# Kernel optimization log

Measured on AMD Instinct MI355X. Metric: run time of the kernel, lower is better.

Reference implementation:

```python
import jax, jax.numpy as jnp
import numpy as np

B, C, H, W = 4, 288, 64, 64
P = 2
HEADS = 36
MLP_RATIO = 4.0
D = C * P * P              # hidden_size = 1152
HF = int(D * MLP_RATIO)    # 4608
LN_EPS = 1e-6
ATTN_EPS = 1e-8


def _layernorm(x):
    # LayerNorm over [C,H,W] per sample, no affine
    mu = jnp.mean(x, axis=(1, 2, 3), keepdims=True)
    var = jnp.mean((x - mu) ** 2, axis=(1, 2, 3), keepdims=True)
    return (x - mu) * jax.lax.rsqrt(var + LN_EPS)


def _seg(x):
    # b c (n1 p) (n2 p) -> b (n1 n2) (c p p)
    b, c, h, w = x.shape
    n1, n2 = h // P, w // P
    x = x.reshape(b, c, n1, P, n2, P).transpose(0, 2, 4, 1, 3, 5)
    return x.reshape(b, n1 * n2, c * P * P)


def _comb(t, h, w):
    # b (n1 n2) (c p p) -> b c (n1 p) (n2 p)
    b, n, dd = t.shape
    n1, n2 = h // P, w // P
    c = dd // (P * P)
    x = t.reshape(b, n1, n2, c, P, P).transpose(0, 3, 1, 4, 2, 5)
    return x.reshape(b, c, h, w)


def _lite_la(t, qkv_w, proj_w, proj_b):
    # ReLU-kernel linear attention with ones-padding normalization trick
    b, s, dm = t.shape
    d = dm // HEADS
    qkv = t @ qkv_w.T                       # [b,s,3*dm]
    q, k, v = jnp.split(qkv, 3, axis=-1)
    q = jax.nn.relu(q).reshape(b, s, HEADS, d)
    k = jax.nn.relu(k).reshape(b, s, HEADS, d)
    v = v.reshape(b, s, HEADS, d)
    v = jnp.concatenate([v, jnp.ones((b, s, HEADS, 1), v.dtype)], axis=-1)  # PAD_VAL=1
    vk = jnp.einsum('bshe,bshd->bhed', v, k)       # [b,h,d+1,d]
    out = jnp.einsum('bhed,bshd->bshe', vk, q)     # [b,s,h,d+1]
    out = out[..., :-1] / (out[..., -1:] + ATTN_EPS)
    return out.reshape(b, s, dm) @ proj_w.T + proj_b


def _glumb(t, inv_w, inv_b, dw_w, dw_b, pw_w):
    # GLU MBConv: 1x1 expand + SiLU -> 3x3 depthwise -> GLU gate -> 1x1 project
    b, n, c = t.shape
    hp = wp = int(n ** 0.5)
    x = t.reshape(b, hp, wp, c).transpose(0, 3, 1, 2)  # NCHW
    x = jnp.einsum('bchw,oc->bohw', x, inv_w[:, :, 0, 0]) + inv_b[None, :, None, None]
    x = jax.nn.silu(x)
    x = jax.lax.conv_general_dilated(x, dw_w, (1, 1), 'SAME',
                                     feature_group_count=dw_w.shape[0],
                                     dimension_numbers=('NCHW', 'OIHW', 'NCHW'))
    x = x + dw_b[None, :, None, None]
    x, gate = jnp.split(x, 2, axis=1)
    x = x * jax.nn.silu(gate)
    x = jnp.einsum('bchw,oc->bohw', x, pw_w[:, :, 0, 0])
    return x.reshape(b, c, n).transpose(0, 2, 1)


def setup_inputs() -> dict:
    key = jax.random.key(0)
    ks = jax.random.split(key, 10)
    s = 0.02
    return {
        'x': jax.random.normal(ks[0], (B, C, H, W), jnp.float32),
        'cond': jax.random.normal(ks[1], (B, 6 * C, H, W), jnp.float32),
        'global_token': jax.random.normal(ks[2], (B, D), jnp.float32),
        'time_token': jax.random.normal(ks[3], (B, D), jnp.float32),
        'ss_w': jax.random.normal(ks[4], (6 * C, 6 * C, 1, 1), jnp.float32) * s,
        'ss_b': jnp.zeros((6 * C,), jnp.float32),
        'qkv_w': jax.random.normal(ks[5], (3 * D, D), jnp.float32) * s,
        'proj_w': jax.random.normal(ks[6], (D, D), jnp.float32) * s,
        'proj_b': jnp.zeros((D,), jnp.float32),
        'inv_w': jax.random.normal(ks[7], (2 * HF, D, 1, 1), jnp.float32) * s,
        'inv_b': jnp.zeros((2 * HF,), jnp.float32),
        'dw_w': jax.random.normal(ks[8], (2 * HF, 1, 3, 3), jnp.float32) * s,
        'dw_b': jnp.zeros((2 * HF,), jnp.float32),
        'pw_w': jax.random.normal(ks[9], (D, HF, 1, 1), jnp.float32) * s,
    }


def reference(x, cond, global_token, time_token, ss_w, ss_b, qkv_w, proj_w, proj_b,
              inv_w, inv_b, dw_w, dw_b, pw_w):
    # scale_shift_table: SiLU + 1x1 conv on cond, chunk into 6 per-channel maps
    ss = jnp.einsum('bchw,oc->bohw', jax.nn.silu(cond), ss_w[:, :, 0, 0]) + ss_b[None, :, None, None]
    sh_msa, sc_msa, g_msa, sh_mlp, sc_mlp, g_mlp = jnp.split(ss, 6, axis=1)
    # attention branch
    tok = _seg(_layernorm(x) * (1.0 + sc_msa) + sh_msa)
    tok = jnp.concatenate([global_token[:, None], time_token[:, None], tok], axis=1)
    a = _lite_la(tok, qkv_w, proj_w, proj_b)
    x = x + _comb(a[:, 2:], H, W) * g_msa
    # MLP branch
    m = _glumb(_seg(_layernorm(x) * (1.0 + sc_mlp) + sh_mlp), inv_w, inv_b, dw_w, dw_b, pw_w)
    x = x + _comb(m, H, W) * g_mlp
    return x
```

## Files before the change

kernel.cpp:

```cpp
#include <hip/hip_runtime.h>
#include <hip/hip_bf16.h>
#include <cstdint>


typedef __bf16 bf16;
typedef bf16 bf16x8 __attribute__((ext_vector_type(8)));
typedef bf16 bf16x4 __attribute__((ext_vector_type(4)));
typedef float f32x4 __attribute__((ext_vector_type(4)));

typedef const __attribute__((address_space(1))) void gas_void;
typedef __attribute__((address_space(3))) void las_void;

__device__ __forceinline__ void gload16(const bf16* g, bf16* l) {
    __builtin_amdgcn_global_load_lds((gas_void*)g, (las_void*)l, 16, 0, 0);
}

#define BB 4
#define CC 288
#define HW 4096
#define C6 1728
#define DD 1152
#define SEQ 1026
#define RTOT 4104
#define NTOK 1024
#define HF 4608
#define HF2 9216
#define NPB 1179648

static constexpr size_t OFF_SUMS = 0;
static constexpr size_t OFF_SS   = 256;
static constexpr size_t SS_BYTES = (size_t)C6 * 16384 * 2;
static constexpr size_t OFF_R2   = OFF_SS + SS_BYTES;
static constexpr size_t OFF_PART1= OFF_R2;
static constexpr size_t OFF_A1   = OFF_R2;
static constexpr size_t OFF_T    = OFF_R2;
static constexpr size_t OFF_QKV  = OFF_T   + (size_t)RTOT*DD*2;
static constexpr size_t OFF_PART2= OFF_QKV;
static constexpr size_t OFF_VK   = OFF_QKV + (size_t)3456*RTOT*2;
static constexpr size_t OFF_ATT  = OFF_VK  + (size_t)144*1056*4;
static constexpr size_t OFF_APROJ= OFF_ATT + (size_t)RTOT*DD*2;
static constexpr size_t OFF_T2   = OFF_R2;
static constexpr size_t OFF_Y    = OFF_T2  + (size_t)4096*DD*2;
static constexpr size_t OFF_G    = OFF_Y   + (size_t)4096*HF2*2;
static constexpr size_t OFF_M    = OFF_G   + (size_t)4096*HF*2;
static constexpr size_t OFF_W    = OFF_R2  + 132120576;
static constexpr size_t OFF_WSS  = OFF_W;
static constexpr size_t OFF_WQKV = OFF_WSS  + (size_t)C6*C6*2;
static constexpr size_t OFF_WPROJ= OFF_WQKV + (size_t)3456*DD*2;
static constexpr size_t OFF_WINV = OFF_WPROJ+ (size_t)DD*DD*2;
static constexpr size_t OFF_WPW  = OFF_WINV + (size_t)HF2*DD*2;

__global__ __launch_bounds__(256) void cvt_bf16(const float* __restrict__ s,
                                                bf16* __restrict__ d, int n4) {
    int i = blockIdx.x * 256 + threadIdx.x;
    if (i < n4) {
        float4 v = ((const float4*)s)[i];
        bf16x4 o = {(bf16)v.x, (bf16)v.y, (bf16)v.z, (bf16)v.w};
        ((bf16x4*)d)[i] = o;
    }
}

__device__ __forceinline__ void block_reduce2_store(float s1, float s2, float* dst) {
    #pragma unroll
    for (int o = 32; o > 0; o >>= 1) { s1 += __shfl_down(s1, o); s2 += __shfl_down(s2, o); }
    __shared__ float r1[4], r2[4];
    int wave = threadIdx.x >> 6, lane = threadIdx.x & 63;
    if (lane == 0) { r1[wave] = s1; r2[wave] = s2; }
    __syncthreads();
    if (threadIdx.x == 0) {
        dst[0] = r1[0] + r1[1] + r1[2] + r1[3];
        dst[1] = r2[0] + r2[1] + r2[2] + r2[3];
    }
}

__global__ __launch_bounds__(256) void ln_stats(const float* __restrict__ x, float* __restrict__ part) {
    const float* base = x + (size_t)blockIdx.x * 4096;
    float s1 = 0.f, s2 = 0.f;
    #pragma unroll
    for (int it = 0; it < 4; it++) {
        float4 v = ((const float4*)base)[it * 256 + threadIdx.x];
        s1 += v.x + v.y + v.z + v.w;
        s2 += v.x * v.x + v.y * v.y + v.z * v.z + v.w * v.w;
    }
    block_reduce2_store(s1, s2, part + (size_t)blockIdx.x * 2);
}

__global__ __launch_bounds__(256) void reduce_part(const float* __restrict__ part, float* __restrict__ sums,
                                                   int nper, int out_off) {
    int b = blockIdx.x;
    float s1 = 0.f, s2 = 0.f;
    for (int i = threadIdx.x; i < nper; i += 256) {
        s1 += part[(size_t)(b * nper + i) * 2];
        s2 += part[(size_t)(b * nper + i) * 2 + 1];
    }
    block_reduce2_store(s1, s2, sums + out_off + b * 2);
}

__global__ __launch_bounds__(256) void prep_cond(const float* __restrict__ cond, bf16* __restrict__ A1) {
    __shared__ float tile[64][65];
    int b = blockIdx.z, k0 = blockIdx.y * 64, h0 = blockIdx.x * 64;
    int col = threadIdx.x & 63, r4 = threadIdx.x >> 6;
    const float* src = cond + ((size_t)b * C6 + k0) * HW + h0;
    #pragma unroll
    for (int p = 0; p < 16; p++) {
        int kk = r4 + p * 4;
        float v = src[(size_t)kk * HW + col];
        tile[col][kk] = v / (1.f + __expf(-v));
    }
    __syncthreads();
    bf16* dst = A1 + ((size_t)(b * HW + h0)) * C6 + k0;
    #pragma unroll
    for (int p = 0; p < 16; p++) {
        int rr = r4 + p * 4;
        dst[(size_t)rr * C6 + col] = (bf16)tile[rr][col];
    }
}

template <int EP, int BIAS>
__global__ __launch_bounds__(256) void gemm_bt(const bf16* __restrict__ A, const bf16* __restrict__ B,
                                               const float* __restrict__ bias, bf16* __restrict__ C,
                                               int M, int N, int K, int reluLimit) {
    __shared__ __align__(16) bf16 As[3][128 * 32];
    __shared__ __align__(16) bf16 Bs[3][128 * 32];
    const int tid = threadIdx.x, wave = tid >> 6, lane = tid & 63;

    const int nx = gridDim.x, ny = gridDim.y, G = 8;
    int idx = blockIdx.y * nx + blockIdx.x;
    int total = nx * ny;
    int q = total >> 3, rm = total & 7;
    int xcd = idx & 7, slot = idx >> 3;
    int vid = (xcd < rm ? xcd * (q + 1) : rm * (q + 1) + (xcd - rm) * q) + slot;
    int band = vid / (G * nx);
    int r = vid - band * (G * nx);
    int gm = min(G, ny - band * G);
    const int m0 = (band * G + r % gm) * 128;
    const int n0 = (r / gm) * 128;

    const int c0 = wave * 128 + lane;
    const int c1 = c0 + 64;
    const int sw = ((c0 >> 2) & 3) ^ ((c0 >> 4) & 3);
    const int ka = (((c0 & 3) ^ sw)) * 8;
    int ra0 = min(m0 + (c0 >> 2), M - 1), ra1 = min(m0 + (c1 >> 2), M - 1);
    int rb0 = min(n0 + (c0 >> 2), N - 1), rb1 = min(n0 + (c1 >> 2), N - 1);
    const bf16* gA0 = A + (size_t)ra0 * K + ka;
    const bf16* gA1 = A + (size_t)ra1 * K + ka;
    const bf16* gB0 = B + (size_t)rb0 * K + ka;
    const bf16* gB1 = B + (size_t)rb1 * K + ka;

    const int wm = (wave >> 1) * 64, wn = (wave & 1) * 64;
    const int l15 = lane & 15;
    const int sr = (l15 & 3) ^ ((l15 >> 2) & 3);
    const int fc = ((lane >> 4) ^ sr) * 8;
    const int fao = (wm + l15) * 32 + fc;
    const int fbo = (wn + l15) * 32 + fc;
    const int lwo = wave * 1024;

    f32x4 acc[4][4];
    #pragma unroll
    for (int i = 0; i < 4; i++)
        #pragma unroll
        for (int j = 0; j < 4; j++) acc[i][j] = (f32x4){0.f, 0.f, 0.f, 0.f};

    auto STAGE = [&](int buf) {
        gload16(gA0, &As[buf][lwo]);
        gload16(gA1, &As[buf][lwo + 512]);
        gload16(gB0, &Bs[buf][lwo]);
        gload16(gB1, &Bs[buf][lwo + 512]);
        gA0 += 32; gA1 += 32; gB0 += 32; gB1 += 32;
    };
    auto COMP = [&](int buf) {
        const bf16* fa = &As[buf][fao];
        const bf16* fb = &Bs[buf][fbo];
        bf16x8 af[4], bv[4];
        #pragma unroll
        for (int i = 0; i < 4; i++) af[i] = *(const bf16x8*)(fa + i * 16 * 32);
        #pragma unroll
        for (int j = 0; j < 4; j++) bv[j] = *(const bf16x8*)(fb + j * 16 * 32);
        #pragma unroll
        for (int i = 0; i < 4; i++)
            #pragma unroll
            for (int j = 0; j < 4; j++)
                acc[i][j] = __builtin_amdgcn_mfma_f32_16x16x32_bf16(af[i], bv[j], acc[i][j], 0, 0, 0);
    };
    auto STEP = [&](int cbuf, int sbuf) {
        STAGE(sbuf);
        asm volatile("s_waitcnt vmcnt(8)" ::: "memory");
        __builtin_amdgcn_s_barrier();
        asm volatile("" ::: "memory");
        COMP(cbuf);
        asm volatile("" ::: "memory");
        __builtin_amdgcn_s_barrier();
    };

    const int nt = K >> 5;
    STAGE(0);
    STAGE(1);
    for (int it = 0; it < nt / 3 - 1; ++it) {
        STEP(0, 2);
        STEP(1, 0);
        STEP(2, 1);
    }
    STEP(0, 2);
    asm volatile("s_waitcnt vmcnt(4)" ::: "memory");
    __builtin_amdgcn_s_barrier();
    asm volatile("" ::: "memory");
    COMP(1);
    asm volatile("" ::: "memory");
    asm volatile("s_waitcnt vmcnt(0)" ::: "memory");
    __builtin_amdgcn_s_barrier();
    asm volatile("" ::: "memory");
    COMP(2);

    const int mq = (lane >> 4) * 4, nl = lane & 15;
    #pragma unroll
    for (int i = 0; i < 4; i++) {
        #pragma unroll
        for (int j = 0; j < 4; j++) {
            int n = n0 + wn + j * 16 + nl;
            if (n < N) {
                #pragma unroll
                for (int r2 = 0; r2 < 4; r2++) {
                    int m = m0 + wm + i * 16 + mq + r2;
                    if (m < M) {
                        float v = acc[i][j][r2];
                        if (BIAS == 1) v += bias[m];
                        else if (BIAS == 2) v += bias[n];
                        if (EP == 1) { if (m < reluLimit) v = fmaxf(v, 0.f); }
                        else if (EP == 2) { v = v / (1.f + __expf(-v)); }
                        C[(size_t)m * N + n] = (bf16)v;
                    }
                }
            }
        }
    }
}

__global__ __launch_bounds__(256) void build_tok_t(const float* __restrict__ xs, const bf16* __restrict__ ss,
                                                   const float* __restrict__ sums, int soff, int shb, int scb,
                                                   bf16* __restrict__ dst, int tokoff, int seqstride) {
    __shared__ bf16 tl[32][132];
    int cch = blockIdx.x, n1 = blockIdx.y, b = blockIdx.z;
    int c0 = cch * 32;
    int tid = threadIdx.x, cl = tid >> 3, wseg = tid & 7;

    float mu = sums[soff + b * 2] * (1.f / (float)NPB);
    float var = sums[soff + b * 2 + 1] * (1.f / (float)NPB) - mu * mu;
    float rsig = rsqrtf(var + 1e-6f);

    int c = c0 + cl;
    #pragma unroll
    for (int hh = 0; hh < 2; hh++) {
        int hw = (2 * n1 + hh) * 64 + wseg * 8;
        const float* xp = xs + ((size_t)b * CC + c) * HW + hw;
        float4 x0 = ((const float4*)xp)[0];
        float4 x1 = ((const float4*)xp)[1];
        bf16x8 scv = *(const bf16x8*)(ss + (size_t)(scb + c) * 16384 + b * HW + hw);
        bf16x8 shv = *(const bf16x8*)(ss + (size_t)(shb + c) * 16384 + b * HW + hw);
        float xv[8] = {x0.x, x0.y, x0.z, x0.w, x1.x, x1.y, x1.z, x1.w};
        #pragma unroll
        for (int k = 0; k < 8; k++) {
            int w = wseg * 8 + k;
            float v = (xv[k] - mu) * rsig * (1.f + (float)scv[k]) + (float)shv[k];
            tl[w >> 1][cl * 4 + hh * 2 + (w & 1)] = (bf16)v;
        }
    }
    __syncthreads();
    int token = tid >> 3, seg = (tid & 7) * 16;
    bf16* drow = dst + ((size_t)(b * seqstride + tokoff + n1 * 32 + token)) * DD + c0 * 4 + seg;
    *(bf16x8*)drow = *(const bf16x8*)&tl[token][seg];
    *(bf16x8*)(drow + 8) = *(const bf16x8*)&tl[token][seg + 8];
}

__global__ __launch_bounds__(256) void copy_gt(const float* __restrict__ gtok, const float* __restrict__ ttok,
                                               bf16* __restrict__ T) {
    int which = blockIdx.x, b = blockIdx.y;
    const float* src = (which == 0 ? gtok : ttok) + b * DD;
    bf16* dst = T + (size_t)(b * SEQ + which) * DD;
    for (int d = threadIdx.x; d < DD; d += 256) dst[d] = (bf16)src[d];
}

__global__ __launch_bounds__(256) void attn_vk(const bf16* __restrict__ qkv, float* __restrict__ vk) {
    int bh = blockIdx.x >> 2, sb = blockIdx.x & 3;
    int b = bh / 36, h = bh % 36;
    int s_begin = sb * 288;
    int s_end = min(s_begin + 288, SEQ);
    const bf16* kbase = qkv + (size_t)(DD + h * 32) * RTOT + b * SEQ;
    const bf16* vbase = qkv + (size_t)(2 * DD + h * 32) * RTOT + b * SEQ;
    __shared__ __align__(16) bf16 kk[32][80];
    __shared__ __align__(16) bf16 vv[32][80];
    int tid = threadIdx.x;
    int e = tid >> 3, dg = (tid & 7) * 4;
    int lrow = tid >> 3, lcol = (tid & 7) * 8;
    float a0 = 0.f, a1 = 0.f, a2 = 0.f, a3 = 0.f, aD = 0.f;
    for (int s0 = s_begin; s0 < s_end; s0 += 64) {
        __syncthreads();
        #pragma unroll
        for (int j = 0; j < 8; j++) {
            int s = s0 + lcol + j;
            bool ok = s < s_end;
            kk[lrow][lcol + j] = ok ? kbase[(size_t)lrow * RTOT + s] : (bf16)0.f;
            vv[lrow][lcol + j] = ok ? vbase[(size_t)lrow * RTOT + s] : (bf16)0.f;
        }
        __syncthreads();
        #pragma unroll
        for (int j0 = 0; j0 < 64; j0 += 8) {
            bf16x8 vvv = *(const bf16x8*)&vv[e][j0];
            bf16x8 k0 = *(const bf16x8*)&kk[dg + 0][j0];
            bf16x8 k1 = *(const bf16x8*)&kk[dg + 1][j0];
            bf16x8 k2 = *(const bf16x8*)&kk[dg + 2][j0];
            bf16x8 k3 = *(const bf16x8*)&kk[dg + 3][j0];
            #pragma unroll
            for (int j = 0; j < 8; j++) {
                float vf = (float)vvv[j];
                a0 += vf * (float)k0[j];
                a1 += vf * (float)k1[j];
                a2 += vf * (float)k2[j];
                a3 += vf * (float)k3[j];
            }
            if (tid < 32) {
                bf16x8 kd = *(const bf16x8*)&kk[tid][j0];
                #pragma unroll
                for (int j = 0; j < 8; j++) aD += (float)kd[j];
            }
        }
    }
    float* dst = vk + (size_t)bh * 1056;
    atomicAdd(&dst[e * 32 + dg + 0], a0);
    atomicAdd(&dst[e * 32 + dg + 1], a1);
    atomicAdd(&dst[e * 32 + dg + 2], a2);
    atomicAdd(&dst[e * 32 + dg + 3], a3);
    if (tid < 32) atomicAdd(&dst[1024 + tid], aD);
}

__global__ __launch_bounds__(256) void attn_out(const bf16* __restrict__ qkv, const float* __restrict__ vk,
                                                bf16* __restrict__ att) {
    int bh = blockIdx.y, b = bh / 36, h = bh % 36;
    int s0 = blockIdx.x * 64;
    __shared__ float vks[1056];
    __shared__ __align__(16) bf16 qs[32][80];
    int tid = threadIdx.x;
    for (int i = tid; i < 1056; i += 256) vks[i] = vk[(size_t)bh * 1056 + i];
    const bf16* qbase = qkv + (size_t)(h * 32) * RTOT + b * SEQ;
    int lrow = tid >> 3, lcol = (tid & 7) * 8;
    #pragma unroll
    for (int j = 0; j < 8; j++) {
        int s = s0 + lcol + j;
        qs[lrow][lcol + j] = (s < SEQ) ? qbase[(size_t)lrow * RTOT + s] : (bf16)0.f;
    }
    __syncthreads();
    int sl = tid >> 2, eg = (tid & 3) * 8;
    int s = s0 + sl;
    float num[8] = {0.f, 0.f, 0.f, 0.f, 0.f, 0.f, 0.f, 0.f};
    float den = 0.f;
    #pragma unroll
    for (int d = 0; d < 32; d++) {
        float qv = (float)qs[d][sl];
        den += vks[1024 + d] * qv;
        #pragma unroll
        for (int t = 0; t < 8; t++) num[t] += vks[(eg + t) * 32 + d] * qv;
    }
    if (s < SEQ) {
        float inv = 1.f / (den + 1e-8f);
        bf16* dst = att + ((size_t)(b * SEQ + s)) * DD + h * 32 + eg;
        #pragma unroll
        for (int t = 0; t < 8; t++) dst[t] = (bf16)(num[t] * inv);
    }
}

__global__ __launch_bounds__(256) void add_attn(const float* __restrict__ x, const bf16* __restrict__ aproj,
                                                const bf16* __restrict__ ss, float* __restrict__ xo,
                                                float* __restrict__ part) {
    int b = blockIdx.x / 4608;
    size_t idx = (size_t)blockIdx.x * 256 + threadIdx.x;
    size_t local = idx - (size_t)b * NPB;
    int c = (int)(local >> 12), hw = (int)(local & 4095);
    int hh = hw >> 6, w = hw & 63;
    int n = (hh >> 1) * 32 + (w >> 1);
    int dd = c * 4 + (hh & 1) * 2 + (w & 1);
    float a = (float)aproj[(size_t)dd * RTOT + b * SEQ + 2 + n];
    float g = (float)ss[(size_t)(576 + c) * 16384 + b * HW + hw];
    float v = x[idx] + a * g;
    xo[idx] = v;
    block_reduce2_store(v, v * v, part + (size_t)blockIdx.x * 2);
}

__global__ __launch_bounds__(256) void dwglu(const bf16* __restrict__ y, const float* __restrict__ dw_w,
                                             const float* __restrict__ dw_b, bf16* __restrict__ g) {
    __shared__ __align__(16) bf16 xs[6400];
    __shared__ __align__(16) bf16 gs[6400];
    int b = blockIdx.z, tile = blockIdx.y, c0 = blockIdx.x * 64;
    int ty = (tile >> 2) * 8, tx = (tile & 3) * 8;
    int tid = threadIdx.x, cc = tid & 63, pg = tid >> 6;
    for (int p = pg; p < 100; p += 4) {
        int py = ty + p / 10 - 1, px = tx + p % 10 - 1;
        bool in = (py >= 0 && py < 32 && px >= 0 && px < 32);
        size_t base = ((size_t)(b * NTOK + py * 32 + px)) * HF2;
        xs[p * 64 + cc] = in ? y[base + c0 + cc] : (bf16)0.f;
        gs[p * 64 + cc] = in ? y[base + HF + c0 + cc] : (bf16)0.f;
    }
    float wx[9], wg[9];
    #pragma unroll
    for (int t = 0; t < 9; t++) {
        wx[t] = dw_w[(size_t)(c0 + cc) * 9 + t];
        wg[t] = dw_w[(size_t)(HF + c0 + cc) * 9 + t];
    }
    float bx = dw_b[c0 + cc], bg = dw_b[HF + c0 + cc];
    __syncthreads();
    for (int p = pg * 16; p < pg * 16 + 16; p++) {
        int py = p >> 3, px = p & 7;
        float ax = bx, ag = bg;
        #pragma unroll
        for (int dy = 0; dy < 3; dy++)
            #pragma unroll
            for (int dx = 0; dx < 3; dx++) {
                int q = (py + dy) * 10 + (px + dx);
                ax += (float)xs[q * 64 + cc] * wx[dy * 3 + dx];
                ag += (float)gs[q * 64 + cc] * wg[dy * 3 + dx];
            }
        float out = ax * (ag / (1.f + __expf(-ag)));
        g[((size_t)(b * NTOK + (ty + py) * 32 + tx + px)) * HF + c0 + cc] = (bf16)out;
    }
}

__global__ __launch_bounds__(256) void add_mlp(const bf16* __restrict__ mm, const bf16* __restrict__ ss,
                                               float* __restrict__ xo) {
    int b = blockIdx.x / 4608;
    size_t idx = (size_t)blockIdx.x * 256 + threadIdx.x;
    size_t local = idx - (size_t)b * NPB;
    int c = (int)(local >> 12), hw = (int)(local & 4095);
    int hh = hw >> 6, w = hw & 63;
    int n = (hh >> 1) * 32 + (w >> 1);
    int dd = c * 4 + (hh & 1) * 2 + (w & 1);
    float mv = (float)mm[(size_t)dd * 4096 + b * NTOK + n];
    float g = (float)ss[(size_t)(1440 + c) * 16384 + b * HW + hw];
    xo[idx] = xo[idx] + mv * g;
}

extern "C" void kernel_launch(void* const* d_in, const int* in_sizes, int n_in,
                              void* d_out, int out_size, void* d_ws, size_t ws_size,
                              hipStream_t stream) {
    (void)in_sizes; (void)n_in; (void)out_size; (void)ws_size;
    const float* x      = (const float*)d_in[0];
    const float* cond   = (const float*)d_in[1];
    const float* gtok   = (const float*)d_in[2];
    const float* ttok   = (const float*)d_in[3];
    const float* ss_w   = (const float*)d_in[4];
    const float* ss_b   = (const float*)d_in[5];
    const float* qkv_w  = (const float*)d_in[6];
    const float* proj_w = (const float*)d_in[7];
    const float* proj_b = (const float*)d_in[8];
    const float* inv_w  = (const float*)d_in[9];
    const float* inv_b  = (const float*)d_in[10];
    const float* dw_w   = (const float*)d_in[11];
    const float* dw_b   = (const float*)d_in[12];
    const float* pw_w   = (const float*)d_in[13];
    float* out = (float*)d_out;
    char* ws = (char*)d_ws;

    float* sums  = (float*)(ws + OFF_SUMS);
    float* PART1 = (float*)(ws + OFF_PART1);
    float* PART2 = (float*)(ws + OFF_PART2);
    bf16* SS    = (bf16*)(ws + OFF_SS);
    bf16* A1    = (bf16*)(ws + OFF_A1);
    bf16* T     = (bf16*)(ws + OFF_T);
    bf16* QKV   = (bf16*)(ws + OFF_QKV);
    float* VK   = (float*)(ws + OFF_VK);
    bf16* ATT   = (bf16*)(ws + OFF_ATT);
    bf16* APROJ = (bf16*)(ws + OFF_APROJ);
    bf16* T2    = (bf16*)(ws + OFF_T2);
    bf16* Y     = (bf16*)(ws + OFF_Y);
    bf16* G     = (bf16*)(ws + OFF_G);
    bf16* MM    = (bf16*)(ws + OFF_M);
    bf16* WSS   = (bf16*)(ws + OFF_WSS);
    bf16* WQKV  = (bf16*)(ws + OFF_WQKV);
    bf16* WPROJ = (bf16*)(ws + OFF_WPROJ);
    bf16* WINV  = (bf16*)(ws + OFF_WINV);
    bf16* WPW   = (bf16*)(ws + OFF_WPW);

    cvt_bf16<<<2916, 256, 0, stream>>>(ss_w, WSS, C6 * C6 / 4);
    cvt_bf16<<<3888, 256, 0, stream>>>(qkv_w, WQKV, 3456 * DD / 4);
    cvt_bf16<<<1296, 256, 0, stream>>>(proj_w, WPROJ, DD * DD / 4);
    cvt_bf16<<<10368, 256, 0, stream>>>(inv_w, WINV, HF2 * DD / 4);
    cvt_bf16<<<5184, 256, 0, stream>>>(pw_w, WPW, DD * HF / 4);

    ln_stats<<<1152, 256, 0, stream>>>(x, PART1);
    reduce_part<<<4, 256, 0, stream>>>(PART1, sums, 288, 0);
    prep_cond<<<dim3(64, 27, 4), 256, 0, stream>>>(cond, A1);
    gemm_bt<0, 1><<<dim3(128, 14), 256, 0, stream>>>(WSS, A1, ss_b, SS, C6, 16384, C6, 0);
    build_tok_t<<<dim3(9, 32, 4), 256, 0, stream>>>(x, SS, sums, 0, 0, 288, T, 2, SEQ);
    copy_gt<<<dim3(2, 4), 256, 0, stream>>>(gtok, ttok, T);
    gemm_bt<1, 0><<<dim3(33, 27), 256, 0, stream>>>(WQKV, T, nullptr, QKV, 3456, RTOT, DD, 2304);
    hipMemsetAsync(ws + OFF_VK, 0, (size_t)144 * 1056 * 4, stream);
    attn_vk<<<576, 256, 0, stream>>>(QKV, VK);
    attn_out<<<dim3(17, 144), 256, 0, stream>>>(QKV, VK, ATT);
    gemm_bt<0, 1><<<dim3(33, 9), 256, 0, stream>>>(WPROJ, ATT, proj_b, APROJ, DD, RTOT, DD, 0);
    add_attn<<<18432, 256, 0, stream>>>(x, APROJ, SS, out, PART2);
    reduce_part<<<4, 256, 0, stream>>>(PART2, sums, 4608, 8);
    build_tok_t<<<dim3(9, 32, 4), 256, 0, stream>>>(out, SS, sums, 8, 864, 1152, T2, 0, 1024);
    gemm_bt<2, 2><<<dim3(72, 32), 256, 0, stream>>>(T2, WINV, inv_b, Y, 4096, HF2, DD, 0);
    dwglu<<<dim3(72, 16, 4), 256, 0, stream>>>(Y, dw_w, dw_b, G);
    gemm_bt<0, 0><<<dim3(32, 9), 256, 0, stream>>>(WPW, G, nullptr, MM, DD, 4096, HF, 0);
    add_mlp<<<18432, 256, 0, stream>>>(MM, SS, out);
}
```

Measured before the change: 960.0 us.

## Add 256x256 tile GEMM with swizzled LDS and interleaved staging for three GEMMs

Adds a new 512-thread GEMM kernel with 256x256 output tiles, K=64 steps, XOR-swizzled LDS layout, double buffering and global loads interleaved between MFMA phases with s_setprio. It replaces the 128x128 GEMM for the scale-shift, QKV and MLP expand projections to raise data reuse per tile and reduce LDS bank conflicts. The dwglu kernel's halo load is also vectorized to 16-byte loads. Larger tiles mean fewer blocks and more wasted work on ragged edges (e.g. M=3456, N=4104), and the kernel uses more registers per thread.

```diff
diff --git a/kernel.cpp b/kernel.cpp
--- a/kernel.cpp
+++ b/kernel.cpp
@@ -117,6 +117,176 @@
 }
 
 template <int EP, int BIAS>
+__global__ __launch_bounds__(512, 2) void gemm256(const bf16* __restrict__ A, const bf16* __restrict__ B,
+                                                  const float* __restrict__ bias, bf16* __restrict__ C,
+                                                  int M, int N, int K, int reluLimit) {
+    __shared__ __align__(16) bf16 As[2][256 * 64];
+    __shared__ __align__(16) bf16 Bs[2][256 * 64];
+    const int tid = threadIdx.x, wave = tid >> 6, lane = tid & 63;
+
+    const int nx = gridDim.x, ny = gridDim.y, G = 8;
+    int idx = blockIdx.y * nx + blockIdx.x;
+    int total = nx * ny;
+    int q = total >> 3, rm = total & 7;
+    int xcd = idx & 7, slot = idx >> 3;
+    int vid = (xcd < rm ? xcd * (q + 1) : rm * (q + 1) + (xcd - rm) * q) + slot;
+    int band = vid / (G * nx);
+    int r = vid - band * (G * nx);
+    int gm = min(G, ny - band * G);
+    const int m0 = (band * G + r % gm) * 256;
+    const int n0 = (r / gm) * 256;
+
+    const int srow_l = (wave << 3) + (lane >> 3);
+    const int sk_el  = (((lane & 7) ^ (lane >> 3)) << 3);
+    const bf16* pA[4]; const bf16* pB[4];
+    #pragma unroll
+    for (int g = 0; g < 4; ++g) {
+        pA[g] = A + (size_t)min(m0 + g * 64 + srow_l, M - 1) * K + sk_el;
+        pB[g] = B + (size_t)min(n0 + g * 64 + srow_l, N - 1) * K + sk_el;
+    }
+    auto STAGE_A = [&](int buf, int half) {
+        #pragma unroll
+        for (int rr = 0; rr < 2; ++rr) {
+            gload16(pA[half * 2 + rr], &As[buf][half * 8192 + rr * 4096 + (wave << 9)]);
+            pA[half * 2 + rr] += 64;
+        }
+    };
+    auto STAGE_B = [&](int buf, int half) {
+        #pragma unroll
+        for (int rr = 0; rr < 2; ++rr) {
+            gload16(pB[half * 2 + rr], &Bs[buf][half * 8192 + rr * 4096 + (wave << 9)]);
+            pB[half * 2 + rr] += 64;
+        }
+    };
+
+    const int wm_w = (wave >> 2) * 128, wn_w = (wave & 3) * 64;
+    const int l15 = lane & 15;
+    const int fswz = (l15 & 7) << 4;
+    const int rk16 = (lane >> 4) << 4;
+
+    bf16x8 af[8], bv[8];
+    f32x4 acc[8][4];
+    #pragma unroll
+    for (int i = 0; i < 8; i++)
+        #pragma unroll
+        for (int j = 0; j < 4; j++) acc[i][j] = (f32x4){0.f, 0.f, 0.f, 0.f};
+
+    auto LDA = [&](const bf16* base, int qm) {
+        #pragma unroll
+        for (int il = 0; il < 4; ++il)
+            #pragma unroll
+            for (int ks = 0; ks < 2; ++ks) {
+                int row = wm_w + (qm * 4 + il) * 16 + l15;
+                int kb  = (ks * 64 + rk16) ^ fswz;
+                af[il * 2 + ks] = *(const bf16x8*)(base + row * 64 + (kb >> 1));
+            }
+    };
+    auto LDB = [&](const bf16* base) {
+        #pragma unroll
+        for (int j = 0; j < 4; ++j)
+            #pragma unroll
+            for (int ks = 0; ks < 2; ++ks) {
+                int row = wn_w + j * 16 + l15;
+                int kb  = (ks * 64 + rk16) ^ fswz;
+                bv[j * 2 + ks] = *(const bf16x8*)(base + row * 64 + (kb >> 1));
+            }
+    };
+    auto MF = [&](int qm, int jh) {
+        __builtin_amdgcn_s_setprio(1);
+        #pragma unroll
+        for (int il = 0; il < 4; ++il)
+            #pragma unroll
+            for (int jl = 0; jl < 2; ++jl)
+                #pragma unroll
+                for (int ks = 0; ks < 2; ++ks)
+                    acc[qm * 4 + il][jh * 2 + jl] = __builtin_amdgcn_mfma_f32_16x16x32_bf16(
+                        af[il * 2 + ks], bv[(jh * 2 + jl) * 2 + ks], acc[qm * 4 + il][jh * 2 + jl], 0, 0, 0);
+        __builtin_amdgcn_s_setprio(0);
+    };
+
+    auto TILE = [&](int t, bool stage_next, bool last_vm) {
+        const int cur = t & 1;
+        const bf16* Ab = &As[cur][0];
+        const bf16* Bb = &Bs[cur][0];
+        LDA(Ab, 0);
+        LDB(Bb);
+        asm volatile("s_waitcnt lgkmcnt(0)" ::: "memory");
+        __builtin_amdgcn_sched_barrier(0);
+        __builtin_amdgcn_s_barrier();
+        MF(0, 0);
+        asm volatile("" ::: "memory");
+        __builtin_amdgcn_s_barrier();
+        asm volatile("" ::: "memory");
+        if (stage_next) STAGE_B(cur, 0);
+        asm volatile("" ::: "memory");
+        __builtin_amdgcn_s_barrier();
+        MF(0, 1);
+        asm volatile("" ::: "memory");
+        __builtin_amdgcn_s_barrier();
+        asm volatile("" ::: "memory");
+        LDA(Ab, 1);
+        if (stage_next) STAGE_B(cur, 1);
+        asm volatile("s_waitcnt lgkmcnt(0)" ::: "memory");
+        __builtin_amdgcn_sched_barrier(0);
+        __builtin_amdgcn_s_barrier();
+        MF(1, 0);
+        asm volatile("" ::: "memory");
+        __builtin_amdgcn_s_barrier();
+        asm volatile("" ::: "memory");
+        if (stage_next) {
+            STAGE_A(cur, 0); STAGE_A(cur, 1);
+            asm volatile("s_waitcnt vmcnt(8)" ::: "memory");
+            __builtin_amdgcn_sched_barrier(0);
+        } else if (last_vm) {
+            asm volatile("s_waitcnt vmcnt(0)" ::: "memory");
+            __builtin_amdgcn_sched_barrier(0);
+        }
+        __builtin_amdgcn_s_barrier();
+        MF(1, 1);
+        asm volatile("" ::: "memory");
+        __builtin_amdgcn_s_barrier();
+        asm volatile("" ::: "memory");
+    };
+
+    const int nt = K >> 6;
+    #pragma unroll
+    for (int tt = 0; tt < 2; ++tt) {
+        STAGE_B(tt, 0); STAGE_B(tt, 1);
+        STAGE_A(tt, 0); STAGE_A(tt, 1);
+    }
+    asm volatile("s_waitcnt vmcnt(8)" ::: "memory");
+    __builtin_amdgcn_sched_barrier(0);
+    __builtin_amdgcn_s_barrier();
+    asm volatile("" ::: "memory");
+    for (int t = 0; t < nt - 2; ++t) TILE(t, true, false);
+    TILE(nt - 2, false, true);
+    TILE(nt - 1, false, false);
+
+    const int mq = (lane >> 4) * 4, nl = lane & 15;
+    #pragma unroll
+    for (int i = 0; i < 8; i++) {
+        #pragma unroll
+        for (int j = 0; j < 4; j++) {
+            int n = n0 + wn_w + j * 16 + nl;
+            if (n < N) {
+                #pragma unroll
+                for (int r2 = 0; r2 < 4; r2++) {
+                    int m = m0 + wm_w + i * 16 + mq + r2;
+                    if (m < M) {
+                        float v = acc[i][j][r2];
+                        if (BIAS == 1) v += bias[m];
+                        else if (BIAS == 2) v += bias[n];
+                        if (EP == 1) { if (m < reluLimit) v = fmaxf(v, 0.f); }
+                        else if (EP == 2) { v = v / (1.f + __expf(-v)); }
+                        C[(size_t)m * N + n] = (bf16)v;
+                    }
+                }
+            }
+        }
+    }
+}
+
+template <int EP, int BIAS>
 __global__ __launch_bounds__(256) void gemm_bt(const bf16* __restrict__ A, const bf16* __restrict__ B,
                                                const float* __restrict__ bias, bf16* __restrict__ C,
                                                int M, int N, int K, int reluLimit) {
@@ -171,16 +341,16 @@
     auto COMP = [&](int buf) {
         const bf16* fa = &As[buf][fao];
         const bf16* fb = &Bs[buf][fbo];
-        bf16x8 af[4], bv[4];
+        bf16x8 af[4], bvv[4];
         #pragma unroll
         for (int i = 0; i < 4; i++) af[i] = *(const bf16x8*)(fa + i * 16 * 32);
         #pragma unroll
-        for (int j = 0; j < 4; j++) bv[j] = *(const bf16x8*)(fb + j * 16 * 32);
+        for (int j = 0; j < 4; j++) bvv[j] = *(const bf16x8*)(fb + j * 16 * 32);
         #pragma unroll
         for (int i = 0; i < 4; i++)
             #pragma unroll
             for (int j = 0; j < 4; j++)
-                acc[i][j] = __builtin_amdgcn_mfma_f32_16x16x32_bf16(af[i], bv[j], acc[i][j], 0, 0, 0);
+                acc[i][j] = __builtin_amdgcn_mfma_f32_16x16x32_bf16(af[i], bvv[j], acc[i][j], 0, 0, 0);
     };
     auto STEP = [&](int cbuf, int sbuf) {
         STAGE(sbuf);
@@ -391,12 +561,24 @@
     int b = blockIdx.z, tile = blockIdx.y, c0 = blockIdx.x * 64;
     int ty = (tile >> 2) * 8, tx = (tile & 3) * 8;
     int tid = threadIdx.x, cc = tid & 63, pg = tid >> 6;
-    for (int p = pg; p < 100; p += 4) {
-        int py = ty + p / 10 - 1, px = tx + p % 10 - 1;
-        bool in = (py >= 0 && py < 32 && px >= 0 && px < 32);
-        size_t base = ((size_t)(b * NTOK + py * 32 + px)) * HF2;
-        xs[p * 64 + cc] = in ? y[base + c0 + cc] : (bf16)0.f;
-        gs[p * 64 + cc] = in ? y[base + HF + c0 + cc] : (bf16)0.f;
+    int pos8 = tid >> 3, cseg = (tid & 7) * 8;
+    bf16x8 z = {(bf16)0.f, (bf16)0.f, (bf16)0.f, (bf16)0.f,
+                (bf16)0.f, (bf16)0.f, (bf16)0.f, (bf16)0.f};
+    #pragma unroll
+    for (int p0 = 0; p0 < 128; p0 += 32) {
+        int p = p0 + pos8;
+        if (p < 100) {
+            int py = ty + p / 10 - 1, px = tx + p % 10 - 1;
+            bool in = (py >= 0 && py < 32 && px >= 0 && px < 32);
+            bf16x8 xv = z, gv = z;
+            if (in) {
+                size_t base = ((size_t)(b * NTOK + py * 32 + px)) * HF2 + c0 + cseg;
+                xv = *(const bf16x8*)&y[base];
+                gv = *(const bf16x8*)&y[base + HF];
+            }
+            *(bf16x8*)&xs[p * 64 + cseg] = xv;
+            *(bf16x8*)&gs[p * 64 + cseg] = gv;
+        }
     }
     float wx[9], wg[9];
     #pragma unroll
@@ -486,10 +668,10 @@
     ln_stats<<<1152, 256, 0, stream>>>(x, PART1);
     reduce_part<<<4, 256, 0, stream>>>(PART1, sums, 288, 0);
     prep_cond<<<dim3(64, 27, 4), 256, 0, stream>>>(cond, A1);
-    gemm_bt<0, 1><<<dim3(128, 14), 256, 0, stream>>>(WSS, A1, ss_b, SS, C6, 16384, C6, 0);
+    gemm256<0, 1><<<dim3(64, 7), 512, 0, stream>>>(WSS, A1, ss_b, SS, C6, 16384, C6, 0);
     build_tok_t<<<dim3(9, 32, 4), 256, 0, stream>>>(x, SS, sums, 0, 0, 288, T, 2, SEQ);
     copy_gt<<<dim3(2, 4), 256, 0, stream>>>(gtok, ttok, T);
-    gemm_bt<1, 0><<<dim3(33, 27), 256, 0, stream>>>(WQKV, T, nullptr, QKV, 3456, RTOT, DD, 2304);
+    gemm256<1, 0><<<dim3(17, 14), 512, 0, stream>>>(WQKV, T, nullptr, QKV, 3456, RTOT, DD, 2304);
     hipMemsetAsync(ws + OFF_VK, 0, (size_t)144 * 1056 * 4, stream);
     attn_vk<<<576, 256, 0, stream>>>(QKV, VK);
     attn_out<<<dim3(17, 144), 256, 0, stream>>>(QKV, VK, ATT);
@@ -497,7 +679,7 @@
     add_attn<<<18432, 256, 0, stream>>>(x, APROJ, SS, out, PART2);
     reduce_part<<<4, 256, 0, stream>>>(PART2, sums, 4608, 8);
     build_tok_t<<<dim3(9, 32, 4), 256, 0, stream>>>(out, SS, sums, 8, 864, 1152, T2, 0, 1024);
-    gemm_bt<2, 2><<<dim3(72, 32), 256, 0, stream>>>(T2, WINV, inv_b, Y, 4096, HF2, DD, 0);
+    gemm256<2, 2><<<dim3(36, 16), 512, 0, stream>>>(T2, WINV, inv_b, Y, 4096, HF2, DD, 0);
     dwglu<<<dim3(72, 16, 4), 256, 0, stream>>>(Y, dw_w, dw_b, G);
     gemm_bt<0, 0><<<dim3(32, 9), 256, 0, stream>>>(WPW, G, nullptr, MM, DD, 4096, HF, 0);
     add_mlp<<<18432, 256, 0, stream>>>(MM, SS, out);
```

New measurement: 1.065 ms. 1.11x slower.
